# Optimization experiments

Measured on AMD Instinct MI355X. Metric: run time of the kernel, lower is better.

The kernel has to match this reference:

```python
import jax, jax.numpy as jnp
import numpy as np
import math

INPUT_SIZE = 2048
HIDDEN_SIZE = 2048
BATCH = 4096


def setup_inputs() -> dict:
    key = jax.random.key(0)
    ks = jax.random.split(key, 16)
    stdv = 1.0 / math.sqrt(HIDDEN_SIZE)

    def u(k, shape):
        return jax.random.uniform(k, shape, jnp.float32, -stdv, stdv)

    inp = {
        "x": jax.random.normal(ks[0], (BATCH, INPUT_SIZE), jnp.float32),
        "h_x": jax.random.normal(ks[1], (BATCH, HIDDEN_SIZE), jnp.float32),
        "c_x": jax.random.normal(ks[2], (BATCH, HIDDEN_SIZE), jnp.float32),
        "W_xi": u(ks[3], (INPUT_SIZE, HIDDEN_SIZE)),
        "W_hi": u(ks[4], (HIDDEN_SIZE, HIDDEN_SIZE)),
        "b_i": u(ks[5], (HIDDEN_SIZE,)),
        "W_xf": u(ks[6], (INPUT_SIZE, HIDDEN_SIZE)),
        "W_hf": u(ks[7], (HIDDEN_SIZE, HIDDEN_SIZE)),
        "b_f": u(ks[8], (HIDDEN_SIZE,)),
        "W_xc": u(ks[9], (INPUT_SIZE, HIDDEN_SIZE)),
        "W_hc": u(ks[10], (HIDDEN_SIZE, HIDDEN_SIZE)),
        "b_c": u(ks[11], (HIDDEN_SIZE,)),
        "W_xo": u(ks[12], (INPUT_SIZE, HIDDEN_SIZE)),
        "W_ho": u(ks[13], (HIDDEN_SIZE, HIDDEN_SIZE)),
        "b_o": u(ks[14], (HIDDEN_SIZE,)),
    }
    return inp


def reference(x, h_x, c_x, W_xi, W_hi, b_i, W_xf, W_hf, b_f, W_xc, W_hc, b_c, W_xo, W_ho, b_o):
    # LSTM cell: 4 gates, each x @ W_x* + h @ W_h* + b_*
    input_gate = jax.nn.sigmoid(x @ W_xi + h_x @ W_hi + b_i)
    forget_gate = jax.nn.sigmoid(x @ W_xf + h_x @ W_hf + b_f)
    output_gate = jax.nn.sigmoid(x @ W_xo + h_x @ W_ho + b_o)
    c_tilda = jnp.tanh(x @ W_xc + h_x @ W_hc + b_c)
    cy = forget_gate * c_x + input_gate * c_tilda
    hy = output_gate * jnp.tanh(cy)
    return (hy, cy)
```

## Files before the change

### kernel.cpp

```cpp
#include <hip/hip_runtime.h>
#include <stdint.h>

typedef __attribute__((ext_vector_type(8))) short short8;
typedef __attribute__((ext_vector_type(8))) unsigned short ushort8;
typedef __attribute__((ext_vector_type(4))) float floatx4;

#define BATCH 4096
#define HID   2048
#define KTOT  4096

__device__ __forceinline__ uint16_t f2bf(float f) {
    union { uint32_t i; float f; } v; v.f = f;
    uint32_t u = v.i;
    u += 0x7fffu + ((u >> 16) & 1u);
    return (uint16_t)(u >> 16);
}
__device__ __forceinline__ float sigmoid_f(float v) {
    return 1.0f / (1.0f + __expf(-v));
}
__device__ __forceinline__ float tanh_f(float v) {
    v = fminf(fmaxf(v, -15.0f), 15.0f);
    float e = __expf(-2.0f * v);
    return (1.0f - e) / (1.0f + e);
}
__device__ __forceinline__ void load_lds16(const uint16_t* g, uint16_t* l) {
    __builtin_amdgcn_global_load_lds(
        (const __attribute__((address_space(1))) void*)g,
        (__attribute__((address_space(3))) void*)l, 16, 0, 0);
}

__global__ __launch_bounds__(256) void conv_w(
    const float* __restrict__ w0, const float* __restrict__ w1,
    const float* __restrict__ w2, const float* __restrict__ w3,
    const float* __restrict__ w4, const float* __restrict__ w5,
    const float* __restrict__ w6, const float* __restrict__ w7,
    uint16_t* __restrict__ wt)
{
    __shared__ uint16_t tile[128 * 128];

    int b   = blockIdx.x;
    int mi  = b >> 8;
    int rem = b & 255;
    int k0  = (rem >> 4) * 128;
    int n0  = (rem & 15) * 128;
    const float* src;
    switch (mi) {
        case 0: src = w0; break; case 1: src = w1; break;
        case 2: src = w2; break; case 3: src = w3; break;
        case 4: src = w4; break; case 5: src = w5; break;
        case 6: src = w6; break; default: src = w7; break;
    }
    int g = mi >> 1, half = mi & 1;
    int ty = threadIdx.x >> 4, tx = threadIdx.x & 15;
    int kr = k0 + ty * 8;
    int nc = n0 + tx * 8;

    ushort8 a[8];
    #pragma unroll
    for (int j = 0; j < 8; ++j) {
        const float* s = src + (size_t)(kr + j) * HID + nc;
        floatx4 f0 = *(const floatx4*)(s);
        floatx4 f1 = *(const floatx4*)(s + 4);
        #pragma unroll
        for (int i = 0; i < 4; ++i) {
            a[j][i]     = f2bf(f0[i]);
            a[j][4 + i] = f2bf(f1[i]);
        }
    }
    ushort8 bt[8];
    #pragma unroll
    for (int i = 0; i < 8; ++i)
        #pragma unroll
        for (int j = 0; j < 8; ++j)
            bt[i][j] = a[j][i];

    #pragma unroll
    for (int i = 0; i < 8; ++i)
        *(ushort8*)(tile + (tx * 8 + i) * 128 + ((ty ^ tx) & 15) * 8) = bt[i];
    __syncthreads();

    int t = threadIdx.x;
    #pragma unroll
    for (int p = 0; p < 8; ++p) {
        int r    = p * 16 + (t >> 4);
        int lc   = t & 15;
        int phys = lc ^ ((r >> 3) & 15);
        ushort8 v = *(const ushort8*)(tile + r * 128 + phys * 8);
        *(ushort8*)(wt + ((size_t)g * HID + n0 + r) * KTOT
                       + half * HID + k0 + lc * 8) = v;
    }
}

__global__ __launch_bounds__(256) void conv_a(
    const float* __restrict__ x, const float* __restrict__ h,
    uint16_t* __restrict__ xh)
{
    size_t base = ((size_t)blockIdx.x * 256 + threadIdx.x) * 8;
    int m = (int)(base >> 12);
    int k = (int)(base & (KTOT - 1));
    const float* s = (k < HID) ? (x + (size_t)m * HID + k)
                               : (h + (size_t)m * HID + (k - HID));
    floatx4 f0 = *(const floatx4*)(s);
    floatx4 f1 = *(const floatx4*)(s + 4);
    ushort8 v;
    #pragma unroll
    for (int j = 0; j < 4; ++j) { v[j] = f2bf(f0[j]); v[4 + j] = f2bf(f1[j]); }
    *(ushort8*)(xh + base) = v;
}

__global__ __launch_bounds__(256, 4) void lstm_gemm_bf16(
    const uint16_t* __restrict__ xh, const float* __restrict__ cx,
    const uint16_t* __restrict__ wt,
    const float* __restrict__ bvi, const float* __restrict__ bvf,
    const float* __restrict__ bvo, const float* __restrict__ bvc,
    float* __restrict__ out)
{
    __shared__ uint16_t ldsA[128 * 64];
    __shared__ uint16_t ldsB[128 * 64];

    int t = threadIdx.x;
    int linear = blockIdx.y * gridDim.x + blockIdx.x;
    int my = (linear & 7) * 4 + ((linear >> 3) & 3);
    int nx = linear >> 5;
    int n0 = nx * 32;
    int m0 = my * 128;

    int wave = t >> 6, lane = t & 63;
    int wr = wave >> 1, wc = wave & 1;
    int lrow = lane & 15, quad = lane >> 4;
    int swz  = lrow & 7;

    int srow = t >> 3;
    int schk = (t & 7) ^ (srow & 7);

    floatx4 acc[4][4] = {};

    for (int kt = 0; kt < KTOT / 64; ++kt) {
        int k0 = kt * 64;

        __syncthreads();
        #pragma unroll
        for (int p = 0; p < 4; ++p) {
            int row = srow + p * 32;
            load_lds16(xh + (size_t)(m0 + row) * KTOT + k0 + schk * 8,
                       ldsA + p * 2048 + t * 8);
        }
        #pragma unroll
        for (int p = 0; p < 4; ++p) {
            int j = srow + p * 32;
            int g = j >> 5, dn = j & 31;
            load_lds16(wt + ((size_t)g * HID + n0 + dn) * KTOT + k0 + schk * 8,
                       ldsB + p * 2048 + t * 8);
        }
        __syncthreads();

        #pragma unroll
        for (int kh = 0; kh < 2; ++kh) {
            int kkc = kh * 4;
            short8 af[4], bfr[4];
            #pragma unroll
            for (int mi = 0; mi < 4; ++mi)
                af[mi] = *(const short8*)(ldsA + (wr * 64 + mi * 16 + lrow) * 64
                                               + (((quad + kkc) ^ swz)) * 8);
            #pragma unroll
            for (int g = 0; g < 4; ++g)
                bfr[g] = *(const short8*)(ldsB + (g * 32 + wc * 16 + lrow) * 64
                                               + (((quad + kkc) ^ swz)) * 8);
            #pragma unroll
            for (int mi = 0; mi < 4; ++mi)
                #pragma unroll
                for (int g = 0; g < 4; ++g)
                    acc[mi][g] = __builtin_amdgcn_mfma_f32_16x16x32_bf16(
                        af[mi], bfr[g], acc[mi][g], 0, 0, 0);
        }
    }

    int col = n0 + wc * 16 + lrow;
    float Bi = bvi[col], Bf = bvf[col], Bo = bvo[col], Bc = bvc[col];
    int rowb = m0 + wr * 64 + quad * 4;

    #pragma unroll
    for (int mi = 0; mi < 4; ++mi) {
        #pragma unroll
        for (int r = 0; r < 4; ++r) {
            int row = rowb + mi * 16 + r;
            size_t off = (size_t)row * HID + col;
            float gi = sigmoid_f(acc[mi][0][r] + Bi);
            float gf = sigmoid_f(acc[mi][1][r] + Bf);
            float go = sigmoid_f(acc[mi][2][r] + Bo);
            float gc = tanh_f   (acc[mi][3][r] + Bc);
            float cyv = gf * cx[off] + gi * gc;
            float hyv = go * tanh_f(cyv);
            out[off] = hyv;
            out[(size_t)BATCH * HID + off] = cyv;
        }
    }
}

__global__ __launch_bounds__(256) void lstm_fused_f32(
    const float* __restrict__ x, const float* __restrict__ h,
    const float* __restrict__ cx,
    const float* __restrict__ wxi, const float* __restrict__ whi,
    const float* __restrict__ wxf, const float* __restrict__ whf,
    const float* __restrict__ wxo, const float* __restrict__ who,
    const float* __restrict__ wxc, const float* __restrict__ whc,
    const float* __restrict__ bvi, const float* __restrict__ bvf,
    const float* __restrict__ bvo, const float* __restrict__ bvc,
    float* __restrict__ out)
{
    __shared__ uint16_t ldsA[128 * 32];
    __shared__ uint16_t ldsB[128 * 32];
    uint32_t* ldsB32 = (uint32_t*)ldsB;

    int t    = threadIdx.x;
    int n0   = blockIdx.x * 32;
    int m0   = blockIdx.y * 128;
    int wave = t >> 6, lane = t & 63;
    int wr = wave >> 1, wc = wave & 1;
    int lrow = lane & 15, quad = lane >> 4;
    int srow = t >> 2;
    int sseg = (t & 3) * 8;
    int gw = wave;
    int ng = lane & 3;
    int ka = lane >> 2;
    const float *wxg, *whg;
    switch (gw) {
        case 0:  wxg = wxi; whg = whi; break;
        case 1:  wxg = wxf; whg = whf; break;
        case 2:  wxg = wxo; whg = who; break;
        default: wxg = wxc; whg = whc; break;
    }

    floatx4 acc[4][4] = {};

    for (int kt = 0; kt < KTOT / 32; ++kt) {
        int k0  = kt * 32;
        int k0h = k0 & (HID - 1);
        bool xhalf = (k0 < HID);

        ushort8 va[2];
        uint32_t bw[8];
        const float* a = xhalf ? x : h;
        #pragma unroll
        for (int p = 0; p < 2; ++p) {
            const float* s = a + (size_t)(m0 + srow + p * 64) * HID + k0h + sseg;
            floatx4 f0 = *(const floatx4*)(s);
            floatx4 f1 = *(const floatx4*)(s + 4);
            #pragma unroll
            for (int j = 0; j < 4; ++j) {
                va[p][j]     = (short)f2bf(f0[j]);
                va[p][4 + j] = (short)f2bf(f1[j]);
            }
        }
        const float* wp  = xhalf ? wxg : whg;
        const float* r0p = wp + (size_t)(k0h + 2 * ka) * HID + n0 + ng * 8;
        floatx4 a0 = *(const floatx4*)(r0p);
        floatx4 a1 = *(const floatx4*)(r0p + 4);
        floatx4 b0 = *(const floatx4*)(r0p + HID);
        floatx4 b1 = *(const floatx4*)(r0p + HID + 4);
        #pragma unroll
        for (int j = 0; j < 4; ++j) {
            bw[j]     = (uint32_t)f2bf(a0[j]) | ((uint32_t)f2bf(b0[j]) << 16);
            bw[4 + j] = (uint32_t)f2bf(a1[j]) | ((uint32_t)f2bf(b1[j]) << 16);
        }

        __syncthreads();
        #pragma unroll
        for (int p = 0; p < 2; ++p)
            *(ushort8*)(ldsA + (srow + p * 64) * 32 + sseg) = va[p];
        #pragma unroll
        for (int j = 0; j < 8; ++j)
            ldsB32[(gw * 32 + ng * 8 + j) * 16 + ka] = bw[j];
        __syncthreads();

        short8 af[4], bfr[4];
        #pragma unroll
        for (int mi = 0; mi < 4; ++mi)
            af[mi] = *(const short8*)(ldsA + (wr * 64 + mi * 16 + lrow) * 32 + quad * 8);
        #pragma unroll
        for (int g = 0; g < 4; ++g)
            bfr[g] = *(const short8*)(ldsB + (g * 32 + wc * 16 + lrow) * 32 + quad * 8);

        #pragma unroll
        for (int mi = 0; mi < 4; ++mi)
            #pragma unroll
            for (int g = 0; g < 4; ++g)
                acc[mi][g] = __builtin_amdgcn_mfma_f32_16x16x32_bf16(
                    af[mi], bfr[g], acc[mi][g], 0, 0, 0);
    }

    int col = n0 + wc * 16 + lrow;
    float Bi = bvi[col], Bf = bvf[col], Bo = bvo[col], Bc = bvc[col];
    int rowb = m0 + wr * 64 + quad * 4;

    #pragma unroll
    for (int mi = 0; mi < 4; ++mi) {
        #pragma unroll
        for (int r = 0; r < 4; ++r) {
            int row = rowb + mi * 16 + r;
            size_t off = (size_t)row * HID + col;
            float gi = sigmoid_f(acc[mi][0][r] + Bi);
            float gf = sigmoid_f(acc[mi][1][r] + Bf);
            float go = sigmoid_f(acc[mi][2][r] + Bo);
            float gc = tanh_f   (acc[mi][3][r] + Bc);
            float cyv = gf * cx[off] + gi * gc;
            float hyv = go * tanh_f(cyv);
            out[off] = hyv;
            out[(size_t)BATCH * HID + off] = cyv;
        }
    }
}

extern "C" void kernel_launch(void* const* d_in, const int* in_sizes, int n_in,
                              void* d_out, int out_size, void* d_ws, size_t ws_size,
                              hipStream_t stream) {
    const float* x    = (const float*)d_in[0];
    const float* h_x  = (const float*)d_in[1];
    const float* c_x  = (const float*)d_in[2];
    const float* W_xi = (const float*)d_in[3];
    const float* W_hi = (const float*)d_in[4];
    const float* b_i  = (const float*)d_in[5];
    const float* W_xf = (const float*)d_in[6];
    const float* W_hf = (const float*)d_in[7];
    const float* b_f  = (const float*)d_in[8];
    const float* W_xc = (const float*)d_in[9];
    const float* W_hc = (const float*)d_in[10];
    const float* b_c  = (const float*)d_in[11];
    const float* W_xo = (const float*)d_in[12];
    const float* W_ho = (const float*)d_in[13];
    const float* b_o  = (const float*)d_in[14];

    const size_t WT_BYTES = (size_t)4 * HID * KTOT * sizeof(uint16_t);
    const size_t XH_BYTES = (size_t)BATCH * KTOT * sizeof(uint16_t);

    if (ws_size >= WT_BYTES + XH_BYTES) {
        uint16_t* wt = (uint16_t*)d_ws;
        uint16_t* xh = (uint16_t*)((char*)d_ws + WT_BYTES);
        hipLaunchKernelGGL(conv_w, dim3(8 * 256), dim3(256), 0, stream,
                           W_xi, W_hi, W_xf, W_hf, W_xo, W_ho, W_xc, W_hc, wt);
        hipLaunchKernelGGL(conv_a, dim3((BATCH * KTOT) / (256 * 8)), dim3(256), 0, stream,
                           x, h_x, xh);
        hipLaunchKernelGGL(lstm_gemm_bf16, dim3(HID / 32, BATCH / 128), dim3(256), 0, stream,
                           xh, c_x, wt, b_i, b_f, b_o, b_c, (float*)d_out);
    } else {
        hipLaunchKernelGGL(lstm_fused_f32, dim3(HID / 32, BATCH / 128), dim3(256), 0, stream,
                           x, h_x, c_x,
                           W_xi, W_hi, W_xf, W_hf, W_xo, W_ho, W_xc, W_hc,
                           b_i, b_f, b_o, b_c, (float*)d_out);
    }
}
```

Measured before the change: 501.9 us.

## Enlarge GEMM tile to 256x256 with double-buffered LDS ping-pong pipeline

```diff
diff --git a/kernel.cpp b/kernel.cpp
--- a/kernel.cpp
+++ b/kernel.cpp
@@ -108,79 +108,121 @@
     *(ushort8*)(xh + base) = v;
 }
 
-__global__ __launch_bounds__(256, 4) void lstm_gemm_bf16(
+
+#define BARRIER() do { asm volatile("" ::: "memory");                         \
+                       __builtin_amdgcn_s_barrier();                          \
+                       __builtin_amdgcn_sched_barrier(0); } while (0)
+#define VM2 asm volatile("s_waitcnt vmcnt(2)" ::: "memory")
+#define VM0 asm volatile("s_waitcnt vmcnt(0)" ::: "memory")
+
+#define STAGE_A(BUF, H, KT) do {                                              \
+    load_lds16(xh + (size_t)(m0 + (H)*128 + srow) * KTOT                      \
+                   + (size_t)(KT)*64 + schk*8,                                \
+               lds + (BUF)*32768 + (H)*8192 + t*8);                           \
+    load_lds16(xh + (size_t)(m0 + (H)*128 + 64 + srow) * KTOT                 \
+                   + (size_t)(KT)*64 + schk*8,                                \
+               lds + (BUF)*32768 + (H)*8192 + 4096 + t*8);                    \
+} while (0)
+
+#define STAGE_B(BUF, H, KT) do {                                              \
+    load_lds16(wt + ((size_t)((H)*2 + 0) * HID + n0 + srow) * KTOT            \
+                   + (size_t)(KT)*64 + schk*8,                                \
+               lds + (BUF)*32768 + 16384 + (H)*8192 + t*8);                   \
+    load_lds16(wt + ((size_t)((H)*2 + 1) * HID + n0 + srow) * KTOT            \
+                   + (size_t)(KT)*64 + schk*8,                                \
+               lds + (BUF)*32768 + 16384 + (H)*8192 + 4096 + t*8);            \
+} while (0)
+
+#define PHASE(BUF, KH, MG, LDB, STAGES, VMW) do {                             \
+    if (LDB) {                                                                \
+      _Pragma("unroll") for (int g_ = 0; g_ < 4; ++g_)                        \
+        bf[g_] = *(const short8*)(lds + (BUF)*32768 + 16384 + boff            \
+                                  + g_*4096 + ((KH) ? pcx1 : pcx0));          \
+    }                                                                         \
+    _Pragma("unroll") for (int m_ = 0; m_ < 4; ++m_)                          \
+      af[m_] = *(const short8*)(lds + (BUF)*32768 + aoff                      \
+                                + ((MG)+m_)*1024 + ((KH) ? pcx1 : pcx0));     \
+    STAGES                                                                    \
+    BARRIER();                                                                \
+    asm volatile("s_waitcnt lgkmcnt(0)" ::: "memory");                        \
+    __builtin_amdgcn_sched_barrier(0);                                        \
+    __builtin_amdgcn_s_setprio(1);                                            \
+    _Pragma("unroll") for (int m_ = 0; m_ < 4; ++m_)                          \
+      _Pragma("unroll") for (int g_ = 0; g_ < 4; ++g_)                        \
+        acc[(MG)+m_][g_] = __builtin_amdgcn_mfma_f32_16x16x32_bf16(           \
+            af[m_], bf[g_], acc[(MG)+m_][g_], 0, 0, 0);                       \
+    __builtin_amdgcn_s_setprio(0);                                            \
+    VMW                                                                       \
+    BARRIER();                                                                \
+} while (0)
+
+__global__ __launch_bounds__(512, 2) void lstm_gemm_bf16(
     const uint16_t* __restrict__ xh, const float* __restrict__ cx,
     const uint16_t* __restrict__ wt,
     const float* __restrict__ bvi, const float* __restrict__ bvf,
     const float* __restrict__ bvo, const float* __restrict__ bvc,
     float* __restrict__ out)
 {
-    __shared__ uint16_t ldsA[128 * 64];
-    __shared__ uint16_t ldsB[128 * 64];
+    __shared__ uint16_t lds[65536];
 
     int t = threadIdx.x;
-    int linear = blockIdx.y * gridDim.x + blockIdx.x;
-    int my = (linear & 7) * 4 + ((linear >> 3) & 3);
-    int nx = linear >> 5;
-    int n0 = nx * 32;
-    int m0 = my * 128;
+
+    int linear = blockIdx.x;
+    int xcd = linear & 7;
+    int idx = linear >> 3;
+    int my  = (xcd >> 2) * 8 + (idx >> 3);
+    int nx  = (xcd & 3) * 8 + (idx & 7);
+    int m0 = my * 256;
+    int n0 = nx * 64;
 
     int wave = t >> 6, lane = t & 63;
-    int wr = wave >> 1, wc = wave & 1;
+    int wr = wave >> 2, wc = wave & 3;
     int lrow = lane & 15, quad = lane >> 4;
     int swz  = lrow & 7;
 
     int srow = t >> 3;
     int schk = (t & 7) ^ (srow & 7);
 
-    floatx4 acc[4][4] = {};
-
-    for (int kt = 0; kt < KTOT / 64; ++kt) {
-        int k0 = kt * 64;
-
-        __syncthreads();
-        #pragma unroll
-        for (int p = 0; p < 4; ++p) {
-            int row = srow + p * 32;
-            load_lds16(xh + (size_t)(m0 + row) * KTOT + k0 + schk * 8,
-                       ldsA + p * 2048 + t * 8);
-        }
-        #pragma unroll
-        for (int p = 0; p < 4; ++p) {
-            int j = srow + p * 32;
-            int g = j >> 5, dn = j & 31;
-            load_lds16(wt + ((size_t)g * HID + n0 + dn) * KTOT + k0 + schk * 8,
-                       ldsB + p * 2048 + t * 8);
-        }
-        __syncthreads();
-
-        #pragma unroll
-        for (int kh = 0; kh < 2; ++kh) {
-            int kkc = kh * 4;
-            short8 af[4], bfr[4];
-            #pragma unroll
-            for (int mi = 0; mi < 4; ++mi)
-                af[mi] = *(const short8*)(ldsA + (wr * 64 + mi * 16 + lrow) * 64
-                                               + (((quad + kkc) ^ swz)) * 8);
-            #pragma unroll
-            for (int g = 0; g < 4; ++g)
-                bfr[g] = *(const short8*)(ldsB + (g * 32 + wc * 16 + lrow) * 64
-                                               + (((quad + kkc) ^ swz)) * 8);
-            #pragma unroll
-            for (int mi = 0; mi < 4; ++mi)
-                #pragma unroll
-                for (int g = 0; g < 4; ++g)
-                    acc[mi][g] = __builtin_amdgcn_mfma_f32_16x16x32_bf16(
-                        af[mi], bfr[g], acc[mi][g], 0, 0, 0);
-        }
+    int aoff = (wr * 128 + lrow) * 64;
+    int boff = (wc * 16 + lrow) * 64;
+    int pcx0 = (quad ^ swz) * 8;
+    int pcx1 = pcx0 ^ 32;
+
+    floatx4 acc[8][4] = {};
+    short8 af[4], bf[4];
+
+    STAGE_B(0, 0, 0);
+    STAGE_B(0, 1, 0);
+    STAGE_A(0, 0, 0);
+    STAGE_A(0, 1, 0);
+    STAGE_B(1, 0, 1);
+    VM2;
+    BARRIER();
+
+    for (int it = 0; it < 32; ++it) {
+        int k1 = 2 * it + 1;
+        int k2 = 2 * it + 2;
+        int k3 = 2 * it + 3;
+        bool st = (it < 31);
+
+        PHASE(0, 0, 0, 1, { STAGE_B(1, 1, k1); }, {});
+        PHASE(0, 0, 4, 0, { STAGE_A(1, 0, k1); }, {});
+        PHASE(0, 1, 0, 1, { STAGE_A(1, 1, k1); }, {});
+        PHASE(0, 1, 4, 0, { if (st) STAGE_B(0, 0, k2); },
+                          { if (st) { VM2; } else { VM0; } });
+        PHASE(1, 0, 0, 1, { if (st) STAGE_B(0, 1, k2); }, {});
+        PHASE(1, 0, 4, 0, { if (st) STAGE_A(0, 0, k2); }, {});
+        PHASE(1, 1, 0, 1, { if (st) STAGE_A(0, 1, k2); }, {});
+        PHASE(1, 1, 4, 0, { if (st) STAGE_B(1, 0, k3); },
+                          { if (st) { VM2; } });
     }
 
     int col = n0 + wc * 16 + lrow;
     float Bi = bvi[col], Bf = bvf[col], Bo = bvo[col], Bc = bvc[col];
-    int rowb = m0 + wr * 64 + quad * 4;
-
-    #pragma unroll
-    for (int mi = 0; mi < 4; ++mi) {
+    int rowb = m0 + wr * 128 + quad * 4;
+
+    #pragma unroll
+    for (int mi = 0; mi < 8; ++mi) {
         #pragma unroll
         for (int r = 0; r < 4; ++r) {
             int row = rowb + mi * 16 + r;
@@ -340,7 +382,7 @@
                            W_xi, W_hi, W_xf, W_hf, W_xo, W_ho, W_xc, W_hc, wt);
         hipLaunchKernelGGL(conv_a, dim3((BATCH * KTOT) / (256 * 8)), dim3(256), 0, stream,
                            x, h_x, xh);
-        hipLaunchKernelGGL(lstm_gemm_bf16, dim3(HID / 32, BATCH / 128), dim3(256), 0, stream,
+        hipLaunchKernelGGL(lstm_gemm_bf16, dim3((BATCH / 256) * (HID / 64)), dim3(512), 0, stream,
                            xh, c_x, wt, b_i, b_f, b_o, b_c, (float*)d_out);
     } else {
         hipLaunchKernelGGL(lstm_fused_f32, dim3(HID / 32, BATCH / 128), dim3(256), 0, stream,
```

Measured after the change: 492.1 us. Within noise of the previous version (-2.0%).
